# Kernel tuning notes

Hardware: AMD Instinct MI355X
Metric: run time of the kernel (lower is better)

## Reference

```python
import jax, jax.numpy as jnp
import numpy as np

B, D, M = 1024, 4096, 128          # batch, input_dim, output_dim (num modules)
HS = [32, 64, 128, 256, 512]       # hidden_dims


def setup_inputs() -> dict:
    key = jax.random.key(0)
    ks = jax.random.split(key, 12)
    inp = {}
    inp["x"] = jax.random.normal(ks[0], (B, D), dtype=jnp.float32)
    # first dense layer: Linear(input_dim, hidden_dims[0]*output_dim)
    inp["W0"] = jax.random.normal(ks[1], (HS[0] * M, D), dtype=jnp.float32) / np.float32(np.sqrt(D))
    inp["b0"] = jnp.zeros((HS[0] * M,), jnp.float32)
    # block-diagonal MaskedLinear layers stored as per-module blocks [M, h_out, h_in]
    for i in range(len(HS) - 1):
        inp[f"W{i+1}"] = jax.random.normal(ks[2 + i], (M, HS[i + 1], HS[i]), dtype=jnp.float32) / np.float32(np.sqrt(HS[i]))
        inp[f"b{i+1}"] = jnp.zeros((M, HS[i + 1]), jnp.float32)
    # output MaskedLinear(h_last, 1, M): blocks [M, 1, h_last] stored as [M, h_last]
    inp["Wout"] = jax.random.normal(ks[10], (M, HS[-1]), dtype=jnp.float32) / np.float32(np.sqrt(HS[-1]))
    inp["bout"] = jnp.zeros((M,), jnp.float32)
    return inp


def reference(x, W0, b0, W1, b1, W2, b2, W3, b3, W4, b4, Wout, bout):
    # Dropout is inference-disabled; MaskedLinear's block-diagonal dense GEMM is
    # computed exactly as a grouped GEMM over the M module blocks (same math,
    # skipping the structurally-zero off-diagonal blocks).
    h = jax.nn.relu(x @ W0.T + b0)                 # [B, M*h0]
    h = h.reshape(x.shape[0], M, HS[0])            # [B, M, h0]
    for W, b in ((W1, b1), (W2, b2), (W3, b3), (W4, b4)):
        h = jax.nn.relu(jnp.einsum('bmi,moi->bmo', h, W) + b)  # [B, M, h_out]
    logits = jnp.einsum('bmi,mi->bm', h, Wout) + bout          # [B, M]
    return jax.nn.sigmoid(logits)
```

## Files before the change

### kernel.cpp

```cpp
#include <hip/hip_runtime.h>
#include <hip/hip_bf16.h>


using bf16 = __hip_bfloat16;
typedef short bf16x8 __attribute__((ext_vector_type(8)));
typedef float f32x4 __attribute__((ext_vector_type(4)));

constexpr int B_ = 1024;
constexpr int M_ = 128;

#define WAITV(N) asm volatile("s_waitcnt vmcnt(" #N ")" ::: "memory")
#define WAITL()  asm volatile("s_waitcnt lgkmcnt(0)" ::: "memory")
#define BAR()    asm volatile("s_barrier" ::: "memory")

__device__ __forceinline__ void gload16_lds(const bf16* gp, bf16* lp) {
    __builtin_amdgcn_global_load_lds(
        (__attribute__((address_space(1))) void*)const_cast<bf16*>(gp),
        (__attribute__((address_space(3))) void*)lp,
        16, 0, 0);
}

struct CvtArgs {
    const float4* src[6];
    short4* dst[6];
};
__global__ void cvt_all(CvtArgs a) {
    constexpr int starts[7] = {0, 1048576, 5242880, 5308416, 5570560,
                               6619136, 10813440};
    int i = blockIdx.x * blockDim.x + threadIdx.x;
    if (i >= starts[6]) return;
    int s = 0;
#pragma unroll
    for (int k = 1; k < 6; ++k) s += (i >= starts[k]) ? 1 : 0;
    int off = i - starts[s];
    float4 v = a.src[s][off];
    union { bf16 h[4]; short4 s4; } u;
    u.h[0] = __float2bfloat16(v.x);
    u.h[1] = __float2bfloat16(v.y);
    u.h[2] = __float2bfloat16(v.z);
    u.h[3] = __float2bfloat16(v.w);
    a.dst[s][off] = u.s4;
}

__global__ __launch_bounds__(256, 2)
void gemm_l0(const bf16* __restrict__ A, const bf16* __restrict__ W,
             const float* __restrict__ bias, bf16* __restrict__ C) {
    constexpr int LDA = 4096;
    __shared__ __align__(16) bf16 sA[2][2][128 * 32];
    __shared__ __align__(16) bf16 sB[2][2][64 * 32];

    const int tid = threadIdx.x, w = tid >> 6, lane = tid & 63;
    const int q = lane >> 4, ln = lane & 15;
    const int lr = lane >> 2, lk = lane & 3;
    const int swz = (lk ^ (lr & 3)) * 8;
    const int wm = w >> 1, wn = w & 1;
    const int r0 = blockIdx.y * 128, c0 = blockIdx.x * 64;

    auto stage = [&](int s, int set) {
        const int k0 = s * 64;
#pragma unroll
        for (int h = 0; h < 2; ++h) {
#pragma unroll
            for (int t = 0; t < 2; ++t) {
                int grp = w * 2 + t;
                gload16_lds(A + (size_t)(r0 + grp * 16 + lr) * LDA + k0 + h * 32 + swz,
                            &sA[set][h][grp * 512]);
            }
            gload16_lds(W + (size_t)(c0 + w * 16 + lr) * LDA + k0 + h * 32 + swz,
                        &sB[set][h][w * 512]);
        }
    };

    f32x4 acc[4][2];
#pragma unroll
    for (int i = 0; i < 4; ++i)
#pragma unroll
        for (int j = 0; j < 2; ++j) acc[i][j] = (f32x4){0.f, 0.f, 0.f, 0.f};

    stage(0, 0);
    stage(1, 1);
    for (int r = 0; r < 64; ++r) {
        if (r < 63) WAITV(6); else WAITV(0);
        BAR();
        const int set = r & 1;
        bf16x8 aF[2][4], bF[2][2];
#pragma unroll
        for (int h = 0; h < 2; ++h) {
#pragma unroll
            for (int i = 0; i < 4; ++i) {
                int row = wm * 64 + i * 16 + ln;
                aF[h][i] = *(const bf16x8*)&sA[set][h][row * 32 + ((q ^ (row & 3)) * 8)];
            }
#pragma unroll
            for (int j = 0; j < 2; ++j) {
                int rn = wn * 32 + j * 16 + ln;
                bF[h][j] = *(const bf16x8*)&sB[set][h][rn * 32 + ((q ^ (rn & 3)) * 8)];
            }
        }
        WAITL();
        BAR();
        if (r + 2 < 64) stage(r + 2, set);
#pragma unroll
        for (int h = 0; h < 2; ++h)
#pragma unroll
            for (int i = 0; i < 4; ++i)
#pragma unroll
                for (int j = 0; j < 2; ++j)
                    acc[i][j] = __builtin_amdgcn_mfma_f32_16x16x32_bf16(
                        aF[h][i], bF[h][j], acc[i][j], 0, 0, 0);
    }

#pragma unroll
    for (int j = 0; j < 2; ++j) {
        int col = c0 + wn * 32 + j * 16 + ln;
        float bv = bias[col];
#pragma unroll
        for (int i = 0; i < 4; ++i)
#pragma unroll
            for (int rr = 0; rr < 4; ++rr) {
                int row = r0 + wm * 64 + i * 16 + q * 4 + rr;
                float v = acc[i][j][rr] + bv;
                v = v > 0.f ? v : 0.f;
                C[(size_t)row * 4096 + col] = __float2bfloat16(v);
            }
    }
}

__global__ __launch_bounds__(256, 2)
void modules_fused(const bf16* __restrict__ h0g,
                   const bf16* __restrict__ W1b, const float* __restrict__ b1,
                   const bf16* __restrict__ W2b, const float* __restrict__ b2,
                   const bf16* __restrict__ W3b, const float* __restrict__ b3,
                   const bf16* __restrict__ W4b, const float* __restrict__ b4,
                   const float* __restrict__ Wout, const float* __restrict__ bout,
                   float* __restrict__ out) {
    constexpr int H3O = 0;
    constexpr int W1B = 8192;
    constexpr int H1O = 10240;
    constexpr int H0O = 16384;
    constexpr int H2O = 16384;
    constexpr int P4B0 = 16384, P4B1 = 20480;
    constexpr int SCO = 16384;
    __shared__ __align__(16) bf16 pool[24576];

    const int tid = threadIdx.x, w = tid >> 6, lane = tid & 63;
    const int q = lane >> 4, ln = lane & 15;
    const int lr = lane >> 2, lk = lane & 3;
    const int swz = (lk ^ (lr & 3)) * 8;
    const int m = blockIdx.y;
    const int r0 = blockIdx.x * 64;

    const bf16* W1m = W1b + (size_t)m * 64 * 32;
    const bf16* W2m = W2b + (size_t)m * 128 * 64;
    const bf16* W3m = W3b + (size_t)m * 256 * 128;
    const bf16* W4m = W4b + (size_t)m * 512 * 256;

    auto stage = [&](const bf16* G, int ldg, int rows, int nr0, int k0, int woff) {
#pragma unroll
        for (int t = 0; t < rows / 64; ++t) {
            int r = t * 64 + w * 16 + lr;
            gload16_lds(G + (size_t)(nr0 + r) * ldg + k0 + swz,
                        pool + woff + t * 2048 + w * 512);
        }
    };
    auto rdA = [&](int hoff, int stride, int row, int kc) -> bf16x8 {
        return *(const bf16x8*)&pool[hoff + row * stride + kc * 8];
    };
    auto rdA0 = [&](int row) -> bf16x8 {
        return *(const bf16x8*)&pool[H0O + row * 32 + ((q ^ (row & 3)) * 8)];
    };
    auto rdB = [&](int woff, int rn) -> bf16x8 {
        return *(const bf16x8*)&pool[woff + rn * 32 + ((q ^ (rn & 3)) * 8)];
    };
    auto wrH = [&](int hoff, int stride, int row, int col, float v) {
        pool[hoff + row * stride + col] = __float2bfloat16(v);
    };
    auto wrH2 = [&](int row, int col, float v) {
        pool[H2O + row * 128 + (((col >> 3) ^ (row & 7)) * 8) + (col & 7)] =
            __float2bfloat16(v);
    };
    auto rdA2 = [&](int row, int kc) -> bf16x8 {
        return *(const bf16x8*)&pool[H2O + row * 128 + ((kc ^ (row & 7)) * 8)];
    };
    auto wrH3 = [&](int row, int col, float v) {
        pool[H3O + row * 256 + (((col >> 3) ^ (row & 7)) * 8) + (col & 7)] =
            __float2bfloat16(v);
    };
    auto rdA3 = [&](int row, int kc) -> bf16x8 {
        return *(const bf16x8*)&pool[H3O + row * 256 + ((kc ^ (row & 7)) * 8)];
    };

    float b1v = b1[m * 64 + w * 16 + ln];
    float b2v[2], b3v[4], b4v[4][2], wov[4][2];
#pragma unroll
    for (int j = 0; j < 2; ++j) b2v[j] = b2[m * 128 + w * 32 + j * 16 + ln];
#pragma unroll
    for (int j = 0; j < 4; ++j) b3v[j] = b3[m * 256 + w * 64 + j * 16 + ln];
#pragma unroll
    for (int nc = 0; nc < 4; ++nc)
#pragma unroll
        for (int j = 0; j < 2; ++j) {
            int col = nc * 128 + w * 32 + j * 16 + ln;
            b4v[nc][j] = b4[(size_t)m * 512 + col];
            wov[nc][j] = Wout[(size_t)m * 512 + col];
        }
    float boutv = bout[m];
    WAITV(0);

    gload16_lds(h0g + (size_t)(r0 + w * 16 + lr) * 4096 + m * 32 + swz,
                pool + H0O + w * 512);
    stage(W1m, 32, 64, 0, 0, W1B);
    stage(W2m, 64, 128, 0, 0, 0);
    stage(W2m, 64, 128, 0, 32, 4096);

    WAITV(4);
    BAR();
    {
        bf16x8 aF[4], bF;
#pragma unroll
        for (int i = 0; i < 4; ++i) aF[i] = rdA0(i * 16 + ln);
        bF = rdB(W1B, w * 16 + ln);
        WAITL();
        BAR();
        f32x4 a1[4];
#pragma unroll
        for (int i = 0; i < 4; ++i) {
            a1[i] = (f32x4){0.f, 0.f, 0.f, 0.f};
            a1[i] = __builtin_amdgcn_mfma_f32_16x16x32_bf16(aF[i], bF, a1[i], 0, 0, 0);
        }
        int col = w * 16 + ln;
#pragma unroll
        for (int i = 0; i < 4; ++i)
#pragma unroll
            for (int rr = 0; rr < 4; ++rr) {
                float v = a1[i][rr] + b1v;
                v = v > 0.f ? v : 0.f;
                wrH(H1O, 72, i * 16 + q * 4 + rr, col, v);
            }
        WAITL();
        BAR();
    }

    {
        f32x4 a2[4][2];
#pragma unroll
        for (int i = 0; i < 4; ++i)
#pragma unroll
            for (int j = 0; j < 2; ++j) a2[i][j] = (f32x4){0.f, 0.f, 0.f, 0.f};
#pragma unroll
        for (int kr = 0; kr < 2; ++kr) {
            if (kr == 0) WAITV(2); else WAITV(0);
            BAR();
            bf16x8 aF[4], bF[2];
#pragma unroll
            for (int i = 0; i < 4; ++i) aF[i] = rdA(H1O, 72, i * 16 + ln, kr * 4 + q);
#pragma unroll
            for (int j = 0; j < 2; ++j) bF[j] = rdB(kr * 4096, w * 32 + j * 16 + ln);
            WAITL();
            BAR();
            if (kr == 1) {
                stage(W3m, 128, 256, 0, 0, 0);
                stage(W3m, 128, 256, 0, 32, 8192);
            }
#pragma unroll
            for (int i = 0; i < 4; ++i)
#pragma unroll
                for (int j = 0; j < 2; ++j)
                    a2[i][j] = __builtin_amdgcn_mfma_f32_16x16x32_bf16(aF[i], bF[j], a2[i][j], 0, 0, 0);
        }
#pragma unroll
        for (int j = 0; j < 2; ++j) {
            int col = w * 32 + j * 16 + ln;
#pragma unroll
            for (int i = 0; i < 4; ++i)
#pragma unroll
                for (int rr = 0; rr < 4; ++rr) {
                    float v = a2[i][j][rr] + b2v[j];
                    v = v > 0.f ? v : 0.f;
                    wrH2(i * 16 + q * 4 + rr, col, v);
                }
        }
        WAITL();
        BAR();
    }

    {
        f32x4 a3[4][4];
#pragma unroll
        for (int i = 0; i < 4; ++i)
#pragma unroll
            for (int j = 0; j < 4; ++j) a3[i][j] = (f32x4){0.f, 0.f, 0.f, 0.f};
#pragma unroll
        for (int kr = 0; kr < 4; ++kr) {
            if (kr < 3) WAITV(4); else WAITV(0);
            BAR();
            bf16x8 aF[4], bF[4];
#pragma unroll
            for (int i = 0; i < 4; ++i) aF[i] = rdA2(i * 16 + ln, kr * 4 + q);
#pragma unroll
            for (int j = 0; j < 4; ++j) bF[j] = rdB((kr & 1) * 8192, w * 64 + j * 16 + ln);
            WAITL();
            BAR();
            if (kr == 0)      stage(W3m, 128, 256, 0, 64, 0);
            else if (kr == 1) stage(W3m, 128, 256, 0, 96, 8192);
            else if (kr == 3) {
                stage(W4m, 256, 128, 0, 0, P4B0);
                stage(W4m, 256, 128, 0, 32, P4B1);
            }
#pragma unroll
            for (int i = 0; i < 4; ++i)
#pragma unroll
                for (int j = 0; j < 4; ++j)
                    a3[i][j] = __builtin_amdgcn_mfma_f32_16x16x32_bf16(aF[i], bF[j], a3[i][j], 0, 0, 0);
        }
#pragma unroll
        for (int j = 0; j < 4; ++j) {
            int col = w * 64 + j * 16 + ln;
#pragma unroll
            for (int i = 0; i < 4; ++i)
#pragma unroll
                for (int rr = 0; rr < 4; ++rr) {
                    float v = a3[i][j][rr] + b3v[j];
                    v = v > 0.f ? v : 0.f;
                    wrH3(i * 16 + q * 4 + rr, col, v);
                }
        }
        WAITL();
        BAR();
    }

    float pl[4][4];
#pragma unroll
    for (int i = 0; i < 4; ++i)
#pragma unroll
        for (int rr = 0; rr < 4; ++rr) pl[i][rr] = 0.f;

#pragma unroll
    for (int nc = 0; nc < 4; ++nc) {
        f32x4 a4[4][2];
#pragma unroll
        for (int i = 0; i < 4; ++i)
#pragma unroll
            for (int j = 0; j < 2; ++j) a4[i][j] = (f32x4){0.f, 0.f, 0.f, 0.f};
#pragma unroll
        for (int kr = 0; kr < 8; ++kr) {
            const int r = nc * 8 + kr;
            if (r < 31) WAITV(2); else WAITV(0);
            BAR();
            const int wb = (r & 1) ? P4B1 : P4B0;
            bf16x8 aF[4], bF[2];
#pragma unroll
            for (int i = 0; i < 4; ++i) aF[i] = rdA3(i * 16 + ln, kr * 4 + q);
#pragma unroll
            for (int j = 0; j < 2; ++j) bF[j] = rdB(wb, w * 32 + j * 16 + ln);
            WAITL();
            BAR();
            if (r + 2 < 32) {
                const int r2 = r + 2;
                stage(W4m, 256, 128, (r2 >> 3) * 128, (r2 & 7) * 32, wb);
            }
#pragma unroll
            for (int i = 0; i < 4; ++i)
#pragma unroll
                for (int j = 0; j < 2; ++j)
                    a4[i][j] = __builtin_amdgcn_mfma_f32_16x16x32_bf16(aF[i], bF[j], a4[i][j], 0, 0, 0);
        }
#pragma unroll
        for (int j = 0; j < 2; ++j) {
            float bb = b4v[nc][j], wv = wov[nc][j];
#pragma unroll
            for (int i = 0; i < 4; ++i)
#pragma unroll
                for (int rr = 0; rr < 4; ++rr) {
                    float v = a4[i][j][rr] + bb;
                    v = v > 0.f ? v : 0.f;
                    pl[i][rr] += v * wv;
                }
        }
    }

    float* sc = (float*)&pool[SCO];
#pragma unroll
    for (int i = 0; i < 4; ++i)
#pragma unroll
        for (int rr = 0; rr < 4; ++rr) {
            float p = pl[i][rr];
            p += __shfl_xor(p, 1);
            p += __shfl_xor(p, 2);
            p += __shfl_xor(p, 4);
            p += __shfl_xor(p, 8);
            if (ln == 0) sc[w * 64 + i * 16 + q * 4 + rr] = p;
        }
    __syncthreads();
    if (tid < 64) {
        float s = sc[tid] + sc[64 + tid] + sc[128 + tid] + sc[192 + tid];
        float lg = s + boutv;
        out[(size_t)(r0 + tid) * M_ + m] = 1.f / (1.f + __expf(-lg));
    }
}

extern "C" void kernel_launch(void* const* d_in, const int* in_sizes, int n_in,
                              void* d_out, int out_size, void* d_ws, size_t ws_size,
                              hipStream_t stream) {
    const float* x    = (const float*)d_in[0];
    const float* W0   = (const float*)d_in[1];
    const float* b0   = (const float*)d_in[2];
    const float* W1   = (const float*)d_in[3];
    const float* b1   = (const float*)d_in[4];
    const float* W2   = (const float*)d_in[5];
    const float* b2   = (const float*)d_in[6];
    const float* W3   = (const float*)d_in[7];
    const float* b3   = (const float*)d_in[8];
    const float* W4   = (const float*)d_in[9];
    const float* b4   = (const float*)d_in[10];
    const float* Wout = (const float*)d_in[11];
    const float* bout = (const float*)d_in[12];
    float* out = (float*)d_out;

    char* ws = (char*)d_ws;
    size_t off = 0;
    auto alloc = [&](size_t bytes) -> void* {
        off = (off + 255) & ~(size_t)255;
        void* p = ws + off;
        off += bytes;
        return p;
    };
    bf16* W0b = (bf16*)alloc((size_t)4096 * 4096 * 2);
    bf16* W1b = (bf16*)alloc((size_t)M_ * 64 * 32 * 2);
    bf16* W2b = (bf16*)alloc((size_t)M_ * 128 * 64 * 2);
    bf16* W3b = (bf16*)alloc((size_t)M_ * 256 * 128 * 2);
    bf16* W4b = (bf16*)alloc((size_t)M_ * 512 * 256 * 2);
    bf16* xb  = (bf16*)alloc((size_t)B_ * 4096 * 2);
    bf16* h0  = (bf16*)alloc((size_t)B_ * 4096 * 2);

    CvtArgs ca;
    ca.src[0] = (const float4*)x;  ca.dst[0] = (short4*)xb;
    ca.src[1] = (const float4*)W0; ca.dst[1] = (short4*)W0b;
    ca.src[2] = (const float4*)W1; ca.dst[2] = (short4*)W1b;
    ca.src[3] = (const float4*)W2; ca.dst[3] = (short4*)W2b;
    ca.src[4] = (const float4*)W3; ca.dst[4] = (short4*)W3b;
    ca.src[5] = (const float4*)W4; ca.dst[5] = (short4*)W4b;
    cvt_all<<<(10813440 + 255) / 256, 256, 0, stream>>>(ca);

    {
        dim3 g(4096 / 64, B_ / 128, 1);
        gemm_l0<<<g, 256, 0, stream>>>(xb, W0b, b0, h0);
    }
    {
        dim3 g(B_ / 64, M_, 1);
        modules_fused<<<g, 256, 0, stream>>>(h0, W1b, b1, W2b, b2, W3b, b3,
                                             W4b, b4, Wout, bout, out);
    }
}
```

Baseline: 328.1 us.

## Stage weights per-wave into private LDS slices to remove block barriers

Reorganizes the LDS layout so each wave stages and reads only its own slice of every weight tile. Because a wave's B-operand buffer is written and read only by that wave, the per-k-step block barriers around weight loads are removed, leaving vmcnt/lgkmcnt waits plus barriers only at activation-layer handoffs. H1 also switches from padded stride-72 to an XOR-swizzled stride-64 layout. The risk is that LDS reuse across phases (W4 buffer overlapping H2, scratch overlapping W4) now depends on fewer barriers being correctly placed.

```diff
diff --git a/kernel.cpp b/kernel.cpp
--- a/kernel.cpp
+++ b/kernel.cpp
@@ -134,13 +134,15 @@
                    const bf16* __restrict__ W4b, const float* __restrict__ b4,
                    const float* __restrict__ Wout, const float* __restrict__ bout,
                    float* __restrict__ out) {
-    constexpr int H3O = 0;
+    constexpr int H2O = 0;
+    constexpr int W4P = 0;
+    constexpr int SCO = 0;
     constexpr int W1B = 8192;
-    constexpr int H1O = 10240;
-    constexpr int H0O = 16384;
-    constexpr int H2O = 16384;
-    constexpr int P4B0 = 16384, P4B1 = 20480;
-    constexpr int SCO = 16384;
+    constexpr int W2B = 10240;
+    constexpr int H0O = 18432;
+    constexpr int H1O = 20480;
+    constexpr int W3P = 8192;
+    constexpr int H3O = 8192;
     __shared__ __align__(16) bf16 pool[24576];
 
     const int tid = threadIdx.x, w = tid >> 6, lane = tid & 63;
@@ -155,25 +157,26 @@
     const bf16* W3m = W3b + (size_t)m * 256 * 128;
     const bf16* W4m = W4b + (size_t)m * 512 * 256;
 
-    auto stage = [&](const bf16* G, int ldg, int rows, int nr0, int k0, int woff) {
-#pragma unroll
-        for (int t = 0; t < rows / 64; ++t) {
-            int r = t * 64 + w * 16 + lr;
-            gload16_lds(G + (size_t)(nr0 + r) * ldg + k0 + swz,
-                        pool + woff + t * 2048 + w * 512);
-        }
-    };
-    auto rdA = [&](int hoff, int stride, int row, int kc) -> bf16x8 {
-        return *(const bf16x8*)&pool[hoff + row * stride + kc * 8];
+    auto stageW = [&](const bf16* G, int ldg, int grow0, int k0, int dstOff,
+                      int nt) {
+#pragma unroll
+        for (int t = 0; t < 4; ++t)
+            if (t < nt)
+                gload16_lds(G + (size_t)(grow0 + t * 16 + lr) * ldg + k0 + swz,
+                            pool + dstOff + t * 512);
+    };
+    auto rdB = [&](int off, int rn) -> bf16x8 {
+        return *(const bf16x8*)&pool[off + rn * 32 + ((q ^ (rn & 3)) * 8)];
     };
     auto rdA0 = [&](int row) -> bf16x8 {
         return *(const bf16x8*)&pool[H0O + row * 32 + ((q ^ (row & 3)) * 8)];
     };
-    auto rdB = [&](int woff, int rn) -> bf16x8 {
-        return *(const bf16x8*)&pool[woff + rn * 32 + ((q ^ (rn & 3)) * 8)];
-    };
-    auto wrH = [&](int hoff, int stride, int row, int col, float v) {
-        pool[hoff + row * stride + col] = __float2bfloat16(v);
+    auto wrH1 = [&](int row, int col, float v) {
+        pool[H1O + row * 64 + (((col >> 3) ^ (row & 7)) * 8) + (col & 7)] =
+            __float2bfloat16(v);
+    };
+    auto rdA1 = [&](int row, int kc) -> bf16x8 {
+        return *(const bf16x8*)&pool[H1O + row * 64 + ((kc ^ (row & 7)) * 8)];
     };
     auto wrH2 = [&](int row, int col, float v) {
         pool[H2O + row * 128 + (((col >> 3) ^ (row & 7)) * 8) + (col & 7)] =
@@ -209,24 +212,19 @@
 
     gload16_lds(h0g + (size_t)(r0 + w * 16 + lr) * 4096 + m * 32 + swz,
                 pool + H0O + w * 512);
-    stage(W1m, 32, 64, 0, 0, W1B);
-    stage(W2m, 64, 128, 0, 0, 0);
-    stage(W2m, 64, 128, 0, 32, 4096);
+    stageW(W1m, 32, w * 16, 0, W1B + w * 512, 1);
+    stageW(W2m, 64, w * 32, 0,  W2B + w * 2048, 2);
+    stageW(W2m, 64, w * 32, 32, W2B + w * 2048 + 1024, 2);
 
     WAITV(4);
     BAR();
     {
-        bf16x8 aF[4], bF;
-#pragma unroll
-        for (int i = 0; i < 4; ++i) aF[i] = rdA0(i * 16 + ln);
-        bF = rdB(W1B, w * 16 + ln);
-        WAITL();
-        BAR();
         f32x4 a1[4];
 #pragma unroll
         for (int i = 0; i < 4; ++i) {
             a1[i] = (f32x4){0.f, 0.f, 0.f, 0.f};
-            a1[i] = __builtin_amdgcn_mfma_f32_16x16x32_bf16(aF[i], bF, a1[i], 0, 0, 0);
+            a1[i] = __builtin_amdgcn_mfma_f32_16x16x32_bf16(
+                rdA0(i * 16 + ln), rdB(W1B + w * 512, ln), a1[i], 0, 0, 0);
         }
         int col = w * 16 + ln;
 #pragma unroll
@@ -234,8 +232,7 @@
 #pragma unroll
             for (int rr = 0; rr < 4; ++rr) {
                 float v = a1[i][rr] + b1v;
-                v = v > 0.f ? v : 0.f;
-                wrH(H1O, 72, i * 16 + q * 4 + rr, col, v);
+                wrH1(i * 16 + q * 4 + rr, col, v > 0.f ? v : 0.f);
             }
         WAITL();
         BAR();
@@ -250,24 +247,23 @@
 #pragma unroll
         for (int kr = 0; kr < 2; ++kr) {
             if (kr == 0) WAITV(2); else WAITV(0);
-            BAR();
             bf16x8 aF[4], bF[2];
 #pragma unroll
-            for (int i = 0; i < 4; ++i) aF[i] = rdA(H1O, 72, i * 16 + ln, kr * 4 + q);
-#pragma unroll
-            for (int j = 0; j < 2; ++j) bF[j] = rdB(kr * 4096, w * 32 + j * 16 + ln);
-            WAITL();
-            BAR();
-            if (kr == 1) {
-                stage(W3m, 128, 256, 0, 0, 0);
-                stage(W3m, 128, 256, 0, 32, 8192);
-            }
+            for (int i = 0; i < 4; ++i) aF[i] = rdA1(i * 16 + ln, kr * 4 + q);
+#pragma unroll
+            for (int j = 0; j < 2; ++j)
+                bF[j] = rdB(W2B + w * 2048 + kr * 1024, j * 16 + ln);
 #pragma unroll
             for (int i = 0; i < 4; ++i)
 #pragma unroll
                 for (int j = 0; j < 2; ++j)
-                    a2[i][j] = __builtin_amdgcn_mfma_f32_16x16x32_bf16(aF[i], bF[j], a2[i][j], 0, 0, 0);
-        }
+                    a2[i][j] = __builtin_amdgcn_mfma_f32_16x16x32_bf16(
+                        aF[i], bF[j], a2[i][j], 0, 0, 0);
+        }
+        WAITL();
+        BAR();
+        stageW(W3m, 128, w * 64, 0,  W3P + w * 4096, 4);
+        stageW(W3m, 128, w * 64, 32, W3P + w * 4096 + 2048, 4);
 #pragma unroll
         for (int j = 0; j < 2; ++j) {
             int col = w * 32 + j * 16 + ln;
@@ -276,8 +272,7 @@
 #pragma unroll
                 for (int rr = 0; rr < 4; ++rr) {
                     float v = a2[i][j][rr] + b2v[j];
-                    v = v > 0.f ? v : 0.f;
-                    wrH2(i * 16 + q * 4 + rr, col, v);
+                    wrH2(i * 16 + q * 4 + rr, col, v > 0.f ? v : 0.f);
                 }
         }
         WAITL();
@@ -293,26 +288,25 @@
 #pragma unroll
         for (int kr = 0; kr < 4; ++kr) {
             if (kr < 3) WAITV(4); else WAITV(0);
-            BAR();
+            const int buf = W3P + w * 4096 + (kr & 1) * 2048;
             bf16x8 aF[4], bF[4];
 #pragma unroll
             for (int i = 0; i < 4; ++i) aF[i] = rdA2(i * 16 + ln, kr * 4 + q);
 #pragma unroll
-            for (int j = 0; j < 4; ++j) bF[j] = rdB((kr & 1) * 8192, w * 64 + j * 16 + ln);
+            for (int j = 0; j < 4; ++j) bF[j] = rdB(buf, j * 16 + ln);
             WAITL();
-            BAR();
-            if (kr == 0)      stage(W3m, 128, 256, 0, 64, 0);
-            else if (kr == 1) stage(W3m, 128, 256, 0, 96, 8192);
-            else if (kr == 3) {
-                stage(W4m, 256, 128, 0, 0, P4B0);
-                stage(W4m, 256, 128, 0, 32, P4B1);
-            }
+            if (kr < 2)
+                stageW(W3m, 128, w * 64, (kr + 2) * 32, buf, 4);
 #pragma unroll
             for (int i = 0; i < 4; ++i)
 #pragma unroll
                 for (int j = 0; j < 4; ++j)
-                    a3[i][j] = __builtin_amdgcn_mfma_f32_16x16x32_bf16(aF[i], bF[j], a3[i][j], 0, 0, 0);
-        }
+                    a3[i][j] = __builtin_amdgcn_mfma_f32_16x16x32_bf16(
+                        aF[i], bF[j], a3[i][j], 0, 0, 0);
+        }
+        BAR();
+        stageW(W4m, 256, w * 32, 0,  W4P + w * 2048, 2);
+        stageW(W4m, 256, w * 32, 32, W4P + w * 2048 + 1024, 2);
 #pragma unroll
         for (int j = 0; j < 4; ++j) {
             int col = w * 64 + j * 16 + ln;
@@ -321,8 +315,7 @@
 #pragma unroll
                 for (int rr = 0; rr < 4; ++rr) {
                     float v = a3[i][j][rr] + b3v[j];
-                    v = v > 0.f ? v : 0.f;
-                    wrH3(i * 16 + q * 4 + rr, col, v);
+                    wrH3(i * 16 + q * 4 + rr, col, v > 0.f ? v : 0.f);
                 }
         }
         WAITL();
@@ -346,24 +339,23 @@
         for (int kr = 0; kr < 8; ++kr) {
             const int r = nc * 8 + kr;
             if (r < 31) WAITV(2); else WAITV(0);
-            BAR();
-            const int wb = (r & 1) ? P4B1 : P4B0;
+            const int buf = W4P + w * 2048 + (r & 1) * 1024;
             bf16x8 aF[4], bF[2];
 #pragma unroll
             for (int i = 0; i < 4; ++i) aF[i] = rdA3(i * 16 + ln, kr * 4 + q);
 #pragma unroll
-            for (int j = 0; j < 2; ++j) bF[j] = rdB(wb, w * 32 + j * 16 + ln);
+            for (int j = 0; j < 2; ++j) bF[j] = rdB(buf, j * 16 + ln);
             WAITL();
-            BAR();
             if (r + 2 < 32) {
                 const int r2 = r + 2;
-                stage(W4m, 256, 128, (r2 >> 3) * 128, (r2 & 7) * 32, wb);
+                stageW(W4m, 256, (r2 >> 3) * 128 + w * 32, (r2 & 7) * 32, buf, 2);
             }
 #pragma unroll
             for (int i = 0; i < 4; ++i)
 #pragma unroll
                 for (int j = 0; j < 2; ++j)
-                    a4[i][j] = __builtin_amdgcn_mfma_f32_16x16x32_bf16(aF[i], bF[j], a4[i][j], 0, 0, 0);
+                    a4[i][j] = __builtin_amdgcn_mfma_f32_16x16x32_bf16(
+                        aF[i], bF[j], a4[i][j], 0, 0, 0);
         }
 #pragma unroll
         for (int j = 0; j < 2; ++j) {
@@ -379,6 +371,7 @@
         }
     }
 
+    BAR();
     float* sc = (float*)&pool[SCO];
 #pragma unroll
     for (int i = 0; i < 4; ++i)
```

Result: faster. 321.5 us (-2.0%).
